# Performance work log

Hardware: AMD Instinct MI355X
Metric: run time of the kernel (lower is better)

Reference implementation:

```python
import jax, jax.numpy as jnp
import numpy as np

# SRU config from the module: 3 layers, highway_bias=0, rescale=True, no layer_norm.
# rescale factor from sru package: sqrt(1 + exp(highway_bias)*2)
SCALE_X = (1.0 + np.exp(0.0) * 2.0) ** 0.5

IMG_DIM, T, HID, NCLS, B = 512, 12, 1024, 51, 2048


def _sru_layer(x, W, vc, b):
    # x: (T, B, d_in); W: (d_in, k*d); vc: (2, d) gate-recurrence vectors; b: (2, d) biases
    Tn, Bn, d_in = x.shape
    d = vc.shape[1]
    k = W.shape[1] // d  # 4 if d_in != d else 3
    U = jnp.einsum('tbi,ij->tbj', x, W).reshape(Tn, Bn, k, d)
    u0, u1, u2 = U[:, :, 0], U[:, :, 1], U[:, :, 2]
    resid = U[:, :, 3] if k == 4 else x  # projected residual when dims differ
    vf, vr = vc[0], vc[1]
    bf, br = b[0], b[1]

    def step(c, inp):
        u0t, u1t, u2t, xt = inp
        f = jax.nn.sigmoid(u1t + vf * c + bf)          # forget gate (uses c_{t-1})
        c_new = f * c + (1.0 - f) * u0t                # cell update
        r = jax.nn.sigmoid(u2t + vr * c_new + br)      # reset gate (uses c_t, as in SRU CUDA)
        h = r * jnp.tanh(c_new) + (1.0 - r) * xt * SCALE_X  # highway with rescale
        return c_new, h

    c0 = jnp.zeros((Bn, d), x.dtype)
    c_last, h = jax.lax.scan(step, c0, (u0, u1, u2, resid))
    return h, c_last


def setup_inputs() -> dict:
    key = jax.random.key(0)
    ks = jax.random.split(key, 12)
    inp = {}
    inp['x'] = jax.random.normal(ks[0], (B, T, IMG_DIM), jnp.float32)
    # layer 0: 512 -> 1024, k=4; layers 1,2: 1024 -> 1024, k=3
    inp['W0'] = jax.random.normal(ks[1], (IMG_DIM, 4 * HID), jnp.float32) / np.sqrt(IMG_DIM)
    inp['W1'] = jax.random.normal(ks[2], (HID, 3 * HID), jnp.float32) / np.sqrt(HID)
    inp['W2'] = jax.random.normal(ks[3], (HID, 3 * HID), jnp.float32) / np.sqrt(HID)
    inp['vc0'] = jax.random.normal(ks[4], (2, HID), jnp.float32) * 0.1
    inp['vc1'] = jax.random.normal(ks[5], (2, HID), jnp.float32) * 0.1
    inp['vc2'] = jax.random.normal(ks[6], (2, HID), jnp.float32) * 0.1
    inp['b0'] = jnp.zeros((2, HID), jnp.float32)
    inp['b1'] = jnp.zeros((2, HID), jnp.float32)
    inp['b2'] = jnp.zeros((2, HID), jnp.float32)
    inp['fc_w'] = jax.random.normal(ks[7], (HID, NCLS), jnp.float32) / np.sqrt(HID)
    inp['fc_b'] = jnp.zeros((NCLS,), jnp.float32)
    return inp


def reference(x, W0, W1, W2, vc0, vc1, vc2, b0, b1, b2, fc_w, fc_b):
    h = jnp.transpose(x, (1, 0, 2))  # (T, B, img_dim)
    for W, vc, b in ((W0, vc0, b0), (W1, vc1, b1), (W2, vc2, b2)):
        h, _ = _sru_layer(h, W, vc, b)
    # dropout layers are identity in eval mode
    logits = jnp.einsum('tbh,hc->tbc', h, fc_w) + fc_b  # (T, B, num_class)
    return jnp.mean(logits, axis=0)  # (B, num_class)
```

## Files before the change

kernel.cpp:

```cpp
#include <hip/hip_runtime.h>
#include <math.h>

#define TSTEPS 12
#define BATCH  2048
#define IMG    512
#define HIDN   1024
#define NCLASS 51
#define SCALE_X 1.7320508075688772f

typedef __attribute__((ext_vector_type(8)))  _Float16 f16x8;
typedef __attribute__((ext_vector_type(2)))  _Float16 f16x2;
typedef __attribute__((ext_vector_type(16))) float    f32x16;

__device__ __forceinline__ float sigf(float x) {
    return 1.f / (1.f + __expf(-x));
}


template<int TJ, int NCOMP>
__global__ __launch_bounds__(256, 2)
void gemm_sru(const _Float16* __restrict__ A, const _Float16* __restrict__ Bt,
              const _Float16* __restrict__ resid,
              const float* __restrict__ vc, const float* __restrict__ bias,
              _Float16* __restrict__ hout, float* __restrict__ hbar, int K) {
    constexpr int BN    = 64 * TJ;
    constexpr int NCH   = BN / NCOMP;
    constexpr int ATILE = 192 * 32;
    constexpr int BTILE = BN * 32;
    constexpr int S_A   = 2 * ATILE;
    constexpr int S_B   = 2 * BTILE;
    constexpr int EPAD  = BN + 8;
    constexpr int EPI   = 96 * EPAD;
    constexpr int HREG  = 96 * NCH;
    constexpr int KTH   = NCH / 16;
    constexpr int PAIRS = NCH / 2;
    constexpr int TOT   = (S_A + S_B) > (EPI + HREG) ? (S_A + S_B) : (EPI + HREG);
    __shared__ __align__(16) _Float16 smem[TOT];

    const int tid  = threadIdx.x;
    const int lane = tid & 63;
    const int w    = tid >> 6;
    const int bm   = blockIdx.y * 192;
    const int bn   = blockIdx.x * BN;
    const int KT   = K >> 4;

    const bool isA = (w < 2);
    const int  nst = isA ? 3 : TJ;
    const _Float16* gsrc = isA ? A : Bt;
    const int rt0g = (isA ? (bm >> 5) : (bn >> 5)) + (w & 1) * nst;
    const _Float16* gbase = gsrc + (size_t)rt0g * KT * 512 + (lane << 3);
    const int lds0  = isA ? 0 : S_A;
    const int ltile = isA ? ATILE : BTILE;
    const int lhalf = (w & 1) * nst * 1024;

    auto stage = [&](int buf, int k0) {
        const _Float16* g = gbase + (size_t)(k0 >> 4) * 512;
        _Float16* l = smem + lds0 + buf * ltile + lhalf;
        for (int i = 0; i < nst; ++i)
            #pragma unroll
            for (int kt = 0; kt < 2; ++kt)
                __builtin_amdgcn_global_load_lds(
                    (const __attribute__((address_space(1))) unsigned int*)(g + ((size_t)i * KT + kt) * 512),
                    (__attribute__((address_space(3))) unsigned int*)(l + (i * 2 + kt) * 512),
                    16, 0, 0);
    };

    const int wy32 = (w >> 1) * 3;
    const int wx32 = (w & 1) * TJ;
    const int l5   = lane >> 5;
    const int m32  = lane & 31;

    f32x16 acc[3][TJ];
    #pragma unroll
    for (int i = 0; i < 3; ++i)
        #pragma unroll
        for (int j = 0; j < TJ; ++j)
            #pragma unroll
            for (int r = 0; r < 16; ++r) acc[i][j][r] = 0.f;

    stage(0, 0);
    int cur = 0;
    for (int k0 = 0; k0 < K; k0 += 32) {
        __syncthreads();
        if (k0 + 32 < K) stage(cur ^ 1, k0 + 32);

        const _Float16* la = smem + cur * ATILE;
        const _Float16* lb = smem + S_A + cur * BTILE;
        #pragma unroll
        for (int ks = 0; ks < 2; ++ks) {
            f16x8 a[3], b[TJ];
            #pragma unroll
            for (int i = 0; i < 3; ++i)
                a[i] = *(const f16x8*)&la[((wy32 + i) * 2 + ks) * 512 + (lane << 3)];
            #pragma unroll
            for (int j = 0; j < TJ; ++j)
                b[j] = *(const f16x8*)&lb[((wx32 + j) * 2 + ks) * 512 + (lane << 3)];
            #pragma unroll
            for (int i = 0; i < 3; ++i)
                #pragma unroll
                for (int j = 0; j < TJ; ++j)
                    acc[i][j] = __builtin_amdgcn_mfma_f32_32x32x16_f16(
                        a[i], b[j], acc[i][j], 0, 0, 0);
        }
        cur ^= 1;
    }

    _Float16 (*uld)[EPAD] = (_Float16 (*)[EPAD])smem;
    _Float16* hreg = smem + EPI;
    const int bl   = tid / PAIRS;
    const int pr   = tid % PAIRS;
    const int gcol = blockIdx.x * NCH + pr * 2;

    #pragma unroll
    for (int pass = 0; pass < 2; ++pass) {
        __syncthreads();
        if ((w >> 1) == pass) {
            #pragma unroll
            for (int i = 0; i < 3; ++i)
                #pragma unroll
                for (int j = 0; j < TJ; ++j)
                    #pragma unroll
                    for (int r = 0; r < 16; ++r) {
                        const int row = i * 32 + (r & 3) + 8 * (r >> 2) + 4 * l5;
                        uld[row][(wx32 + j) * 32 + m32] = (_Float16)acc[i][j][r];
                    }
        }
        __syncthreads();

        if (tid < 8 * PAIRS) {
            const float2 vf  = *(const float2*)&vc[gcol];
            const float2 vr  = *(const float2*)&vc[HIDN + gcol];
            const float2 bfv = *(const float2*)&bias[gcol];
            const float2 brv = *(const float2*)&bias[HIDN + gcol];
            const int ca = (pr * 2) * NCOMP, cb = (pr * 2 + 1) * NCOMP;

            float c0 = 0.f, c1 = 0.f, s0 = 0.f, s1 = 0.f;
            #pragma unroll
            for (int t = 0; t < TSTEPS; ++t) {
                const int row = bl * 12 + t;
                const float u0a = (float)uld[row][ca + 0];
                const float u1a = (float)uld[row][ca + 1];
                const float u2a = (float)uld[row][ca + 2];
                const float u0b = (float)uld[row][cb + 0];
                const float u1b = (float)uld[row][cb + 1];
                const float u2b = (float)uld[row][cb + 2];
                float xta, xtb;
                if (NCOMP == 4) {
                    xta = (float)uld[row][ca + 3];
                    xtb = (float)uld[row][cb + 3];
                } else {
                    const int grow = bm + pass * 96 + row;
                    const size_t gran = ((size_t)(grow >> 5) * KT + (gcol >> 4)) * 512
                                      + (size_t)((grow & 31) + ((gcol >> 3) & 1) * 32) * 8
                                      + (gcol & 7);
                    const f16x2 xv = *(const f16x2*)&resid[gran];
                    xta = (float)xv[0]; xtb = (float)xv[1];
                }

                const float f0 = sigf(u1a + vf.x * c0 + bfv.x);
                c0 = f0 * c0 + (1.f - f0) * u0a;
                const float r0_ = sigf(u2a + vr.x * c0 + brv.x);
                const float th0 = 2.f * sigf(2.f * c0) - 1.f;
                const float hv0 = r0_ * th0 + (1.f - r0_) * xta * SCALE_X;

                const float f1 = sigf(u1b + vf.y * c1 + bfv.y);
                c1 = f1 * c1 + (1.f - f1) * u0b;
                const float r1_ = sigf(u2b + vr.y * c1 + brv.y);
                const float th1 = 2.f * sigf(2.f * c1) - 1.f;
                const float hv1 = r1_ * th1 + (1.f - r1_) * xtb * SCALE_X;

                if (hout) {
                    const int rtl  = row >> 5;
                    const int ktl  = pr >> 3;
                    const int lloc = (row & 31) + ((pr >> 2) & 1) * 32;
                    f16x2 hv = { (_Float16)hv0, (_Float16)hv1 };
                    *(f16x2*)&hreg[(rtl * KTH + ktl) * 512 + lloc * 8 + (pr & 3) * 2] = hv;
                }
                s0 += hv0; s1 += hv1;
            }
            if (hbar) {
                const int gb = bm / 12 + pass * 8 + bl;
                *(float2*)&hbar[(size_t)gb * HIDN + gcol] =
                    make_float2(s0 * (1.f / TSTEPS), s1 * (1.f / TSTEPS));
            }
        }

        if (hout) {
            __syncthreads();
            const int rtg0 = (bm + pass * 96) >> 5;
            for (int g = tid; g < HREG / 8; g += 256) {
                const int c = g >> 6, l = g & 63;
                const f16x8 v = *(const f16x8*)&hreg[c * 512 + l * 8];
                const int rtl = c / KTH, ktl = c % KTH;
                const size_t gc = (size_t)(rtg0 + rtl) * 64 + blockIdx.x * KTH + ktl;
                *(f16x8*)&hout[gc * 512 + l * 8] = v;
            }
        }
    }
}

template<int NC>
__global__ __launch_bounds__(256)
void wsplit_t(const float* __restrict__ W, _Float16* __restrict__ Wt, int K) {
    const int N  = NC * 1024;
    const int KT = K >> 4;
    const int g  = blockIdx.x * 256 + threadIdx.x;
    const int c  = g >> 6, l = g & 63;
    const int rt = c / KT, kt = c - rt * KT;
    const int np = rt * 32 + (l & 31);
    const int h  = np / NC, comp = np - h * NC;
    const int n  = comp * 1024 + h;
    const int k  = (kt << 4) + ((l >> 5) << 3);
    f16x8 v;
    #pragma unroll
    for (int j = 0; j < 8; ++j)
        v[j] = (_Float16)W[(size_t)(k + j) * N + n];
    *(f16x8*)&Wt[(size_t)g * 8] = v;
}

__global__ __launch_bounds__(256)
void esplit(const float* __restrict__ src, _Float16* __restrict__ dst) {
    const int g  = blockIdx.x * 256 + threadIdx.x;
    const int c  = g >> 6, l = g & 63;
    const int rt = c >> 5, kt = c & 31;
    const int row = rt * 32 + (l & 31);
    const int k   = (kt << 4) + ((l >> 5) << 3);
    const float4 v0 = *(const float4*)&src[(size_t)row * 512 + k];
    const float4 v1 = *(const float4*)&src[(size_t)row * 512 + k + 4];
    f16x8 v = { (_Float16)v0.x, (_Float16)v0.y, (_Float16)v0.z, (_Float16)v0.w,
                (_Float16)v1.x, (_Float16)v1.y, (_Float16)v1.z, (_Float16)v1.w };
    *(f16x8*)&dst[(size_t)g * 8] = v;
}

__global__ __launch_bounds__(64)
void final_fc(const float* __restrict__ hbar, const float* __restrict__ fcw,
              const float* __restrict__ fcb, float* __restrict__ out) {
    __shared__ float hrow[HIDN];
    const int b = blockIdx.x;
    for (int i = threadIdx.x; i < HIDN; i += 64)
        hrow[i] = hbar[(size_t)b * HIDN + i];
    __syncthreads();

    const int c = threadIdx.x;
    if (c < NCLASS) {
        float acc = fcb[c];
        #pragma unroll 8
        for (int k = 0; k < HIDN; ++k)
            acc = fmaf(hrow[k], fcw[(size_t)k * NCLASS + c], acc);
        out[(size_t)b * NCLASS + c] = acc;
    }
}

extern "C" void kernel_launch(void* const* d_in, const int* in_sizes, int n_in,
                              void* d_out, int out_size, void* d_ws, size_t ws_size,
                              hipStream_t stream) {
    const float* x   = (const float*)d_in[0];
    const float* W0  = (const float*)d_in[1];
    const float* W1  = (const float*)d_in[2];
    const float* W2  = (const float*)d_in[3];
    const float* vc0 = (const float*)d_in[4];
    const float* vc1 = (const float*)d_in[5];
    const float* vc2 = (const float*)d_in[6];
    const float* b0  = (const float*)d_in[7];
    const float* b1  = (const float*)d_in[8];
    const float* b2  = (const float*)d_in[9];
    const float* fcw = (const float*)d_in[10];
    const float* fcb = (const float*)d_in[11];
    float* out = (float*)d_out;

    char* ws = (char*)d_ws;
    size_t off = 0;
    auto carve = [&](size_t bytes) { char* p = ws + off; off = (off + bytes + 255) & ~255ull; return p; };

    _Float16* W0t = (_Float16*)carve((size_t)4096 * 512 * 2);
    _Float16* W1t = (_Float16*)carve((size_t)3072 * 1024 * 2);
    _Float16* W2t = (_Float16*)carve((size_t)3072 * 1024 * 2);
    const size_t W_BYTES = off;

    const size_t PER_B = 12ull * 512 * 2 + 2ull * 12 * 1024 * 2 + 1024ull * 4 + 1024;
    int CB = 32;
    if      (W_BYTES + 2048ull * PER_B <= ws_size) CB = 2048;
    else if (W_BYTES + 1024ull * PER_B <= ws_size) CB = 1024;
    else if (W_BYTES +  512ull * PER_B <= ws_size) CB = 512;
    else if (W_BYTES +  256ull * PER_B <= ws_size) CB = 256;
    else if (W_BYTES +  128ull * PER_B <= ws_size) CB = 128;
    else if (W_BYTES +   64ull * PER_B <= ws_size) CB = 64;
    const int MC = CB * TSTEPS;

    _Float16* x16  = (_Float16*)carve((size_t)MC * 512 * 2);
    _Float16* hA16 = (_Float16*)carve((size_t)MC * 1024 * 2);
    _Float16* hB16 = (_Float16*)carve((size_t)MC * 1024 * 2);
    float*    hbar = (float*)carve((size_t)CB * 1024 * 4);

    const dim3 blk256(256);

    wsplit_t<4><<<dim3((4096 / 32) * (512 / 16) * 64 / 256),  blk256, 0, stream>>>(W0, W0t, 512);
    wsplit_t<3><<<dim3((3072 / 32) * (1024 / 16) * 64 / 256), blk256, 0, stream>>>(W1, W1t, 1024);
    wsplit_t<3><<<dim3((3072 / 32) * (1024 / 16) * 64 / 256), blk256, 0, stream>>>(W2, W2t, 1024);

    for (int cb = 0; cb < BATCH / CB; ++cb) {
        const float* xc   = x   + (size_t)cb * CB * TSTEPS * IMG;
        float*       outc = out + (size_t)cb * CB * NCLASS;

        esplit<<<dim3(MC / 4), blk256, 0, stream>>>(xc, x16);
        gemm_sru<2, 4><<<dim3(4096 / 128, MC / 192), blk256, 0, stream>>>(
            x16, W0t, nullptr, vc0, b0, hA16, nullptr, 512);

        gemm_sru<3, 3><<<dim3(3072 / 192, MC / 192), blk256, 0, stream>>>(
            hA16, W1t, hA16, vc1, b1, hB16, nullptr, 1024);

        gemm_sru<3, 3><<<dim3(3072 / 192, MC / 192), blk256, 0, stream>>>(
            hB16, W2t, hB16, vc2, b2, nullptr, hbar, 1024);

        final_fc<<<dim3(CB), dim3(64), 0, stream>>>(hbar, fcw, fcb, outc);
    }
}
```

Baseline: 764.4 us.

## Triple-buffer GEMM loads, swizzle block order, and tile-transpose weight and input packing

```diff
diff --git a/kernel.cpp b/kernel.cpp
--- a/kernel.cpp
+++ b/kernel.cpp
@@ -16,40 +16,50 @@
     return 1.f / (1.f + __expf(-x));
 }
 
+#define VMCNT_IMM(n) (0x0F70 | (n))
+
 
 template<int TJ, int NCOMP>
 __global__ __launch_bounds__(256, 2)
 void gemm_sru(const _Float16* __restrict__ A, const _Float16* __restrict__ Bt,
               const _Float16* __restrict__ resid,
               const float* __restrict__ vc, const float* __restrict__ bias,
-              _Float16* __restrict__ hout, float* __restrict__ hbar, int K) {
+              _Float16* __restrict__ hout, float* __restrict__ hbar, int K,
+              int pcshift) {
     constexpr int BN    = 64 * TJ;
     constexpr int NCH   = BN / NCOMP;
     constexpr int ATILE = 192 * 32;
     constexpr int BTILE = BN * 32;
-    constexpr int S_A   = 2 * ATILE;
-    constexpr int S_B   = 2 * BTILE;
+    constexpr int S_A3  = 3 * ATILE;
     constexpr int EPAD  = BN + 8;
     constexpr int EPI   = 96 * EPAD;
     constexpr int HREG  = 96 * NCH;
     constexpr int KTH   = NCH / 16;
     constexpr int PAIRS = NCH / 2;
-    constexpr int TOT   = (S_A + S_B) > (EPI + HREG) ? (S_A + S_B) : (EPI + HREG);
+    constexpr int STG   = 3 * (ATILE + BTILE);
+    constexpr int TOT   = STG > (EPI + HREG) ? STG : (EPI + HREG);
     __shared__ __align__(16) _Float16 smem[TOT];
 
     const int tid  = threadIdx.x;
     const int lane = tid & 63;
     const int w    = tid >> 6;
-    const int bm   = blockIdx.y * 192;
-    const int bn   = blockIdx.x * BN;
-    const int KT   = K >> 4;
+
+    const int nbx = gridDim.x;
+    const int b   = blockIdx.y * nbx + blockIdx.x;
+    const int pc1 = (nbx >> 3) - 1;
+    const int xk  = b & 7, s = b >> 3;
+    const int bx  = xk + ((s & pc1) << 3);
+    const int by  = s >> pcshift;
+
+    const int bm  = by * 192;
+    const int KT  = K >> 4;
 
     const bool isA = (w < 2);
     const int  nst = isA ? 3 : TJ;
     const _Float16* gsrc = isA ? A : Bt;
-    const int rt0g = (isA ? (bm >> 5) : (bn >> 5)) + (w & 1) * nst;
+    const int rt0g = (isA ? (bm >> 5) : (bx * (BN >> 5))) + (w & 1) * nst;
     const _Float16* gbase = gsrc + (size_t)rt0g * KT * 512 + (lane << 3);
-    const int lds0  = isA ? 0 : S_A;
+    const int lds0  = isA ? 0 : S_A3;
     const int ltile = isA ? ATILE : BTILE;
     const int lhalf = (w & 1) * nst * 1024;
 
@@ -79,37 +89,47 @@
             for (int r = 0; r < 16; ++r) acc[i][j][r] = 0.f;
 
     stage(0, 0);
-    int cur = 0;
+    stage(1, 32);
+    int bi = 0;
     for (int k0 = 0; k0 < K; k0 += 32) {
-        __syncthreads();
-        if (k0 + 32 < K) stage(cur ^ 1, k0 + 32);
-
-        const _Float16* la = smem + cur * ATILE;
-        const _Float16* lb = smem + S_A + cur * BTILE;
+        if (k0 + 32 < K) {
+            if (isA) __builtin_amdgcn_s_waitcnt(VMCNT_IMM(6));
+            else     __builtin_amdgcn_s_waitcnt(VMCNT_IMM(2 * TJ));
+        } else {
+            __builtin_amdgcn_s_waitcnt(VMCNT_IMM(0));
+        }
+        __builtin_amdgcn_s_barrier();
+        if (k0 + 64 < K) {
+            int nb = bi + 2; if (nb >= 3) nb -= 3;
+            stage(nb, k0 + 64);
+        }
+
+        const _Float16* la = smem + bi * ATILE;
+        const _Float16* lb = smem + S_A3 + bi * BTILE;
         #pragma unroll
         for (int ks = 0; ks < 2; ++ks) {
-            f16x8 a[3], b[TJ];
+            f16x8 a[3], bfr[TJ];
             #pragma unroll
             for (int i = 0; i < 3; ++i)
                 a[i] = *(const f16x8*)&la[((wy32 + i) * 2 + ks) * 512 + (lane << 3)];
             #pragma unroll
             for (int j = 0; j < TJ; ++j)
-                b[j] = *(const f16x8*)&lb[((wx32 + j) * 2 + ks) * 512 + (lane << 3)];
+                bfr[j] = *(const f16x8*)&lb[((wx32 + j) * 2 + ks) * 512 + (lane << 3)];
             #pragma unroll
             for (int i = 0; i < 3; ++i)
                 #pragma unroll
                 for (int j = 0; j < TJ; ++j)
                     acc[i][j] = __builtin_amdgcn_mfma_f32_32x32x16_f16(
-                        a[i], b[j], acc[i][j], 0, 0, 0);
-        }
-        cur ^= 1;
+                        a[i], bfr[j], acc[i][j], 0, 0, 0);
+        }
+        ++bi; if (bi == 3) bi = 0;
     }
 
     _Float16 (*uld)[EPAD] = (_Float16 (*)[EPAD])smem;
     _Float16* hreg = smem + EPI;
     const int bl   = tid / PAIRS;
     const int pr   = tid % PAIRS;
-    const int gcol = blockIdx.x * NCH + pr * 2;
+    const int gcol = bx * NCH + pr * 2;
 
     #pragma unroll
     for (int pass = 0; pass < 2; ++pass) {
@@ -192,7 +212,7 @@
                 const int c = g >> 6, l = g & 63;
                 const f16x8 v = *(const f16x8*)&hreg[c * 512 + l * 8];
                 const int rtl = c / KTH, ktl = c % KTH;
-                const size_t gc = (size_t)(rtg0 + rtl) * 64 + blockIdx.x * KTH + ktl;
+                const size_t gc = (size_t)(rtg0 + rtl) * 64 + bx * KTH + ktl;
                 *(f16x8*)&hout[gc * 512 + l * 8] = v;
             }
         }
@@ -202,34 +222,64 @@
 template<int NC>
 __global__ __launch_bounds__(256)
 void wsplit_t(const float* __restrict__ W, _Float16* __restrict__ Wt, int K) {
+    __shared__ _Float16 tile[32][132];
     const int N  = NC * 1024;
     const int KT = K >> 4;
-    const int g  = blockIdx.x * 256 + threadIdx.x;
-    const int c  = g >> 6, l = g & 63;
-    const int rt = c / KT, kt = c - rt * KT;
-    const int np = rt * 32 + (l & 31);
+    const int rt = blockIdx.x, kc = blockIdx.y;
+
+    const int nl = threadIdx.x & 31;
+    const int kl = threadIdx.x >> 5;
+    const int np = rt * 32 + nl;
     const int h  = np / NC, comp = np - h * NC;
     const int n  = comp * 1024 + h;
-    const int k  = (kt << 4) + ((l >> 5) << 3);
-    f16x8 v;
-    #pragma unroll
-    for (int j = 0; j < 8; ++j)
-        v[j] = (_Float16)W[(size_t)(k + j) * N + n];
-    *(f16x8*)&Wt[(size_t)g * 8] = v;
+    #pragma unroll
+    for (int kk = 0; kk < 16; ++kk) {
+        const int k = kc * 128 + kl * 16 + kk;
+        tile[nl][kl * 16 + kk] = (_Float16)W[(size_t)k * N + n];
+    }
+    __syncthreads();
+
+    #pragma unroll
+    for (int p = 0; p < 2; ++p) {
+        const int slot = p * 256 + threadIdx.x;
+        const int ktl  = slot >> 6, l = slot & 63;
+        f16x8 v;
+        #pragma unroll
+        for (int j = 0; j < 8; ++j)
+            v[j] = tile[l & 31][ktl * 16 + ((l >> 5) << 3) + j];
+        const int kt = kc * 8 + ktl;
+        *(f16x8*)&Wt[((size_t)rt * KT + kt) * 512 + l * 8] = v;
+    }
 }
 
 __global__ __launch_bounds__(256)
 void esplit(const float* __restrict__ src, _Float16* __restrict__ dst) {
-    const int g  = blockIdx.x * 256 + threadIdx.x;
-    const int c  = g >> 6, l = g & 63;
-    const int rt = c >> 5, kt = c & 31;
-    const int row = rt * 32 + (l & 31);
-    const int k   = (kt << 4) + ((l >> 5) << 3);
-    const float4 v0 = *(const float4*)&src[(size_t)row * 512 + k];
-    const float4 v1 = *(const float4*)&src[(size_t)row * 512 + k + 4];
-    f16x8 v = { (_Float16)v0.x, (_Float16)v0.y, (_Float16)v0.z, (_Float16)v0.w,
-                (_Float16)v1.x, (_Float16)v1.y, (_Float16)v1.z, (_Float16)v1.w };
-    *(f16x8*)&dst[(size_t)g * 8] = v;
+    __shared__ _Float16 tile[32][132];
+    const int rt = blockIdx.x, kc = blockIdx.y;
+    const int kli = threadIdx.x & 31;
+    const int rl  = threadIdx.x >> 5;
+    #pragma unroll
+    for (int rr = 0; rr < 4; ++rr) {
+        const int row = rl * 4 + rr;
+        const float4 v = *(const float4*)&src[(size_t)(rt * 32 + row) * 512 + kc * 128 + kli * 4];
+        tile[row][kli * 4 + 0] = (_Float16)v.x;
+        tile[row][kli * 4 + 1] = (_Float16)v.y;
+        tile[row][kli * 4 + 2] = (_Float16)v.z;
+        tile[row][kli * 4 + 3] = (_Float16)v.w;
+    }
+    __syncthreads();
+
+    #pragma unroll
+    for (int p = 0; p < 2; ++p) {
+        const int slot = p * 256 + threadIdx.x;
+        const int ktl  = slot >> 6, l = slot & 63;
+        f16x8 v;
+        #pragma unroll
+        for (int j = 0; j < 8; ++j)
+            v[j] = tile[l & 31][ktl * 16 + ((l >> 5) << 3) + j];
+        const int kt = kc * 8 + ktl;
+        *(f16x8*)&dst[((size_t)rt * 32 + kt) * 512 + l * 8] = v;
+    }
 }
 
 __global__ __launch_bounds__(64)
@@ -294,23 +344,23 @@
 
     const dim3 blk256(256);
 
-    wsplit_t<4><<<dim3((4096 / 32) * (512 / 16) * 64 / 256),  blk256, 0, stream>>>(W0, W0t, 512);
-    wsplit_t<3><<<dim3((3072 / 32) * (1024 / 16) * 64 / 256), blk256, 0, stream>>>(W1, W1t, 1024);
-    wsplit_t<3><<<dim3((3072 / 32) * (1024 / 16) * 64 / 256), blk256, 0, stream>>>(W2, W2t, 1024);
+    wsplit_t<4><<<dim3(4096 / 32, 512 / 128),  blk256, 0, stream>>>(W0, W0t, 512);
+    wsplit_t<3><<<dim3(3072 / 32, 1024 / 128), blk256, 0, stream>>>(W1, W1t, 1024);
+    wsplit_t<3><<<dim3(3072 / 32, 1024 / 128), blk256, 0, stream>>>(W2, W2t, 1024);
 
     for (int cb = 0; cb < BATCH / CB; ++cb) {
         const float* xc   = x   + (size_t)cb * CB * TSTEPS * IMG;
         float*       outc = out + (size_t)cb * CB * NCLASS;
 
-        esplit<<<dim3(MC / 4), blk256, 0, stream>>>(xc, x16);
+        esplit<<<dim3(MC / 32, 4), blk256, 0, stream>>>(xc, x16);
         gemm_sru<2, 4><<<dim3(4096 / 128, MC / 192), blk256, 0, stream>>>(
-            x16, W0t, nullptr, vc0, b0, hA16, nullptr, 512);
+            x16, W0t, nullptr, vc0, b0, hA16, nullptr, 512, 2);
 
         gemm_sru<3, 3><<<dim3(3072 / 192, MC / 192), blk256, 0, stream>>>(
-            hA16, W1t, hA16, vc1, b1, hB16, nullptr, 1024);
+            hA16, W1t, hA16, vc1, b1, hB16, nullptr, 1024, 1);
 
         gemm_sru<3, 3><<<dim3(3072 / 192, MC / 192), blk256, 0, stream>>>(
-            hB16, W2t, hB16, vc2, b2, nullptr, hbar, 1024);
+            hB16, W2t, hB16, vc2, b2, nullptr, hbar, 1024, 1);
 
         final_fc<<<dim3(CB), dim3(64), 0, stream>>>(hbar, fcw, fcb, outc);
     }
```

Measured after the change: 776.3 us. Within noise of the previous version (+1.5%).
